# Kernel tuning notes

Measured on AMD Instinct MI355X. Metric: run time of the kernel, lower is better.

Reference implementation:

```python
import jax, jax.numpy as jnp
import numpy as np

B, T = 32, 2048            # batch, seq_len
V = 16                     # vocab_size
H = 256                    # hidden_size
NV = V + 2                 # embedding rows (padding_idx=0 + vocab + delimiter)
NO = V + 1                 # head output size


def setup_inputs() -> dict:
    key = jax.random.key(0)
    ks = jax.random.split(key, 8)
    s = 1.0 / np.sqrt(H).astype(np.float32)
    tokens = jax.random.randint(ks[0], (B, T), 0, NV)
    embed = jax.random.normal(ks[1], (NV, H), jnp.float32) * 0.02
    embed = embed.at[0].set(0.0)  # padding_idx=0
    # GRU params (PyTorch layout: gates [r|z|n] stacked on last dim)
    W_ih = jax.random.uniform(ks[2], (H, 3 * H), jnp.float32, -s, s)
    W_hh = jax.random.uniform(ks[3], (H, 3 * H), jnp.float32, -s, s)
    b_ih = jax.random.uniform(ks[4], (3 * H,), jnp.float32, -s, s)
    b_hh = jax.random.uniform(ks[5], (3 * H,), jnp.float32, -s, s)
    W_head = jax.random.uniform(ks[6], (H, NO), jnp.float32, -s, s)
    b_head = jax.random.uniform(ks[7], (NO,), jnp.float32, -s, s)
    return {"tokens": tokens, "embed": embed, "W_ih": W_ih, "W_hh": W_hh,
            "b_ih": b_ih, "b_hh": b_hh, "W_head": W_head, "b_head": b_head}


def _mogru_scan(x, W_ih, W_hh, b_ih, b_hh):
    # x: [B, T, H]. Precompute all input projections in one big GEMM.
    gi = x @ W_ih + b_ih                      # [B, T, 3H]
    gi_t = jnp.swapaxes(gi, 0, 1)             # [T, B, 3H] for scan
    h0 = jnp.zeros((x.shape[0], W_hh.shape[0]), x.dtype)

    def step(h, gi_step):
        gh = h @ W_hh + b_hh                  # [B, 3H]
        i_r, i_z, i_n = jnp.split(gi_step, 3, axis=-1)
        h_r, h_z, h_n = jnp.split(gh, 3, axis=-1)
        r = jax.nn.sigmoid(i_r + h_r)
        z = jax.nn.sigmoid(i_z + h_z)         # beta: retention gate
        n = jnp.tanh(i_n + r * h_n)
        h_new = (1.0 - z) * n + z * h
        return h_new, (h_new, z)

    h_last, (outs, betas) = jax.lax.scan(step, h0, gi_t)
    return jnp.swapaxes(outs, 0, 1), h_last, jnp.swapaxes(betas, 0, 1)


def reference(tokens, embed, W_ih, W_hh, b_ih, b_hh, W_head, b_head):
    x = embed[tokens]                          # [B, T, H] embedding lookup
    output, _, betas = _mogru_scan(x, W_ih, W_hh, b_ih, b_hh)
    logits = output @ W_head + b_head          # [B, T, V+1]
    return logits, betas
```

## Files before the change

### kernel.cpp

```cpp
#include <hip/hip_runtime.h>

#define BB   32
#define TT   2048
#define HH   256
#define G3   768
#define NVOC 18
#define NOUT 17
#define LOGITS_ELEMS ((size_t)BB * TT * NOUT)

typedef _Float16 h2 __attribute__((ext_vector_type(2)));

__device__ __forceinline__ float bf1(unsigned short u){
  union{unsigned int i; float f;} v; v.i = ((unsigned int)u) << 16; return v.f;
}
__device__ __forceinline__ unsigned short f2bf(float f){
  union{float f; unsigned int i;} v; v.f = f;
  unsigned int lsb = (v.i >> 16) & 1u;
  v.i += 0x7fffu + lsb;
  return (unsigned short)(v.i >> 16);
}
__device__ __forceinline__ float bflo(unsigned int u){
  union{unsigned int i; float f;} v; v.i = u << 16; return v.f;
}
__device__ __forceinline__ float bfhi(unsigned int u){
  union{unsigned int i; float f;} v; v.i = u & 0xffff0000u; return v.f;
}

__device__ __forceinline__ float ld1(const float* p, size_t i){ return p[i]; }
__device__ __forceinline__ float ld1(const unsigned short* p, size_t i){ return bf1(p[i]); }

__device__ __forceinline__ bool detect_f32(const void* W_ih_raw){
  const unsigned short* u = (const unsigned short*)W_ih_raw;
  bool big = false;
  #pragma unroll
  for (int i = 0; i < 64; i++){
    float v = bf1(u[i]);
    big |= !(v >= -0.25f && v <= 0.25f);
  }
  return big;
}

#if __has_builtin(__builtin_amdgcn_fdot2)
#define FDOT2(a,b,c) __builtin_amdgcn_fdot2((a),(b),(c),false)
#else
#define FDOT2(a,b,c) ((c) + (float)(a).x*(float)(b).x + (float)(a).y*(float)(b).y)
#endif

template<typename T>
__device__ __forceinline__ void prep_body(const T* W_hh, unsigned int* Wp){
  unsigned int e = blockIdx.x * 256 + threadIdx.x;
  unsigned int c = e & 3, tmp = e >> 2;
  unsigned int tid = tmp & 511, f = tmp >> 9;
  unsigned int m = (f << 2) | c;
  unsigned int g = m >> 6, kk = m & 63;
  unsigned int u = tid >> 1, q = tid & 1;
  unsigned int col = g * 256 + u;
  unsigned int k0 = q * 128 + kk * 2;
  float lo = ld1(W_hh, (size_t)k0 * G3 + col);
  float hi = ld1(W_hh, (size_t)(k0 + 1) * G3 + col);
  h2 t; t.x = (_Float16)lo; t.y = (_Float16)hi;
  Wp[e] = __builtin_bit_cast(unsigned int, t);
}

__global__ __launch_bounds__(256) void k_prep(
    const void* __restrict__ W_hh, const void* __restrict__ W_ih,
    unsigned int* __restrict__ Wp)
{
  if (detect_f32(W_ih)) prep_body<float>((const float*)W_hh, Wp);
  else                  prep_body<unsigned short>((const unsigned short*)W_hh, Wp);
}

template<typename T>
__device__ __forceinline__ void proj_body(const T* embed, const T* W_ih,
                                          const T* b_ih, const T* b_hh,
                                          float* proj, float* bb){
  __shared__ float s_e[HH];
  int v = blockIdx.x, j = threadIdx.x;
  if (j < HH) s_e[j] = ld1(embed, (size_t)v * HH + j);
  if (v == 0) bb[j] = ld1(b_hh, (size_t)j);
  __syncthreads();
  float acc = ld1(b_ih, (size_t)j);
  if (j < 2 * HH) acc += ld1(b_hh, (size_t)j);
  #pragma unroll 8
  for (int k = 0; k < HH; k++)
    acc += s_e[k] * ld1(W_ih, (size_t)k * G3 + j);
  proj[(size_t)v * G3 + j] = acc;
}

__global__ __launch_bounds__(768) void k_proj(
    const void* __restrict__ embed, const void* __restrict__ W_ih,
    const void* __restrict__ b_ih, const void* __restrict__ b_hh,
    float* __restrict__ proj, float* __restrict__ bb)
{
  if (detect_f32(W_ih))
    proj_body<float>((const float*)embed, (const float*)W_ih,
                     (const float*)b_ih, (const float*)b_hh, proj, bb);
  else
    proj_body<unsigned short>((const unsigned short*)embed,
                              (const unsigned short*)W_ih,
                              (const unsigned short*)b_ih,
                              (const unsigned short*)b_hh, proj, bb);
}

#define SPROJ_PAD 6656

__global__ __launch_bounds__(512, 1)
__attribute__((amdgpu_waves_per_eu(1, 2)))
void k_scan(
    const int*          __restrict__ tokens,
    const unsigned int* __restrict__ Wp,
    const float*        __restrict__ bb,
    const void*         __restrict__ W_ih,
    const float*        __restrict__ proj,
    unsigned short*     __restrict__ outs,
    void*               __restrict__ d_out_base)
{
  __shared__ float s_proj[NVOC * G3 + SPROJ_PAD];
  __shared__ __align__(16) unsigned int s_hA[136];
  __shared__ __align__(16) unsigned int s_hB[136];

  const bool f32m = detect_f32(W_ih);
  const int b   = blockIdx.x;
  const int tid = threadIdx.x;
  const int u   = tid >> 1;
  const int q   = tid & 1;

  for (int i = tid; i < NVOC * G3; i += 512) s_proj[i] = proj[i];

  h2 w[192];
  {
    const float4* wp4 = (const float4*)Wp;
    #pragma unroll
    for (int f = 0; f < 48; f++) {
      float4 v = wp4[(size_t)f * 512 + tid];
      w[4*f+0] = __builtin_bit_cast(h2, v.x);
      w[4*f+1] = __builtin_bit_cast(h2, v.y);
      w[4*f+2] = __builtin_bit_cast(h2, v.z);
      w[4*f+3] = __builtin_bit_cast(h2, v.w);
    }
  }
  const float bbn = bb[2 * HH + u];

  if (tid < 136) s_hA[tid] = 0u;
  float h_old = 0.f;

  const int* tptr = tokens + (size_t)b * TT;
  int tok = tptr[0];
  unsigned short* orow   = outs + (size_t)b * TT * HH + u;
  unsigned short* brow_b = (unsigned short*)d_out_base + LOGITS_ELEMS
                           + (size_t)b * TT * HH + u;
  float*          brow_f = (float*)d_out_base + LOGITS_ELEMS
                           + (size_t)b * TT * HH + u;

  __syncthreads();

#define STEP(T, RB, WB)                                                      \
  {                                                                          \
    int tok_cur = tok;                                                       \
    tok = ((T) + 1 < TT) ? tptr[(T) + 1] : 0;                                \
    const float* pj = s_proj + tok_cur * G3;                                 \
    float gir = pj[u], giz = pj[HH + u], gin = pj[2*HH + u];                 \
    const int4* hp = (const int4*)(RB);                                      \
    float ar[4] = {0.f,0.f,0.f,0.f};                                         \
    float az[4] = {0.f,0.f,0.f,0.f};                                         \
    float an[4] = {0.f,0.f,0.f,0.f};                                         \
    _Pragma("unroll")                                                        \
    for (int i = 0; i < 16; i++) {                                           \
      int4 hv = hp[q * 17 + i];                                              \
      h2 x0 = __builtin_bit_cast(h2, hv.x);                                  \
      h2 x1 = __builtin_bit_cast(h2, hv.y);                                  \
      h2 x2 = __builtin_bit_cast(h2, hv.z);                                  \
      h2 x3 = __builtin_bit_cast(h2, hv.w);                                  \
      ar[0] = FDOT2(w[4*i+0],       x0, ar[0]);                              \
      ar[1] = FDOT2(w[4*i+1],       x1, ar[1]);                              \
      ar[2] = FDOT2(w[4*i+2],       x2, ar[2]);                              \
      ar[3] = FDOT2(w[4*i+3],       x3, ar[3]);                              \
      az[0] = FDOT2(w[64+4*i+0],    x0, az[0]);                              \
      az[1] = FDOT2(w[64+4*i+1],    x1, az[1]);                              \
      az[2] = FDOT2(w[64+4*i+2],    x2, az[2]);                              \
      az[3] = FDOT2(w[64+4*i+3],    x3, az[3]);                              \
      an[0] = FDOT2(w[128+4*i+0],   x0, an[0]);                              \
      an[1] = FDOT2(w[128+4*i+1],   x1, an[1]);                              \
      an[2] = FDOT2(w[128+4*i+2],   x2, an[2]);                              \
      an[3] = FDOT2(w[128+4*i+3],   x3, an[3]);                              \
    }                                                                        \
    float gr = (ar[0] + ar[1]) + (ar[2] + ar[3]);                            \
    float gz = (az[0] + az[1]) + (az[2] + az[3]);                            \
    float gn = (an[0] + an[1]) + (an[2] + an[3]);                            \
    gr += __shfl_xor(gr, 1);                                                 \
    gz += __shfl_xor(gz, 1);                                                 \
    gn += __shfl_xor(gn, 1);                                                 \
    float r = 1.f / (1.f + __expf(-(gir + gr)));                             \
    float z = 1.f / (1.f + __expf(-(giz + gz)));                             \
    float x = gin + r * (gn + bbn);                                          \
    x = fminf(fmaxf(x, -15.f), 15.f);                                        \
    float ex = __expf(2.f * x);                                              \
    float n = (ex - 1.f) / (ex + 1.f);                                       \
    float hn = (1.f - z) * n + z * h_old;                                    \
    h_old = hn;                                                              \
    if (q == 0) {                                                            \
      ((_Float16*)(WB))[(u >> 7) * 136 + (u & 127)] = (_Float16)hn;          \
      orow[(size_t)(T) * HH] = f2bf(hn);                                     \
    } else {                                                                 \
      if (f32m) brow_f[(size_t)(T) * HH] = z;                                \
      else      brow_b[(size_t)(T) * HH] = f2bf(z);                          \
    }                                                                        \
    __syncthreads();                                                         \
  }

  for (int t = 0; t < TT; t += 2) {
    STEP(t,     s_hA, s_hB)
    STEP(t + 1, s_hB, s_hA)
  }
#undef STEP
}

template<typename T>
__device__ __forceinline__ void stage_head(const T* W_head, const T* b_head,
                                           float* s_w, float* s_b, int tid){
  for (int i = tid; i < NOUT * HH; i += 256) {
    int o = i / HH, k = i - o * HH;
    s_w[i] = ld1(W_head, (size_t)k * NOUT + o);
  }
  if (tid < NOUT) s_b[tid] = ld1(b_head, (size_t)tid);
}

__global__ __launch_bounds__(256) void k_head(
    const unsigned short* __restrict__ outs,
    const void* __restrict__ W_head,
    const void* __restrict__ b_head,
    const void* __restrict__ W_ih,
    void* __restrict__ logits_out)
{
  __shared__ float s_w[NOUT * HH];
  __shared__ float s_b[NOUT];
  const bool f32m = detect_f32(W_ih);
  const int tid = threadIdx.x;

  if (f32m) stage_head<float>((const float*)W_head, (const float*)b_head,
                              s_w, s_b, tid);
  else      stage_head<unsigned short>((const unsigned short*)W_head,
                                       (const unsigned short*)b_head,
                                       s_w, s_b, tid);
  __syncthreads();

  size_t gid = (size_t)blockIdx.x * 256 + tid;
  if (gid >= LOGITS_ELEMS) return;
  int o = (int)(gid % NOUT);
  size_t row = gid / NOUT;

  const uint4* xp = (const uint4*)(outs + row * HH);
  const float* wv = s_w + o * HH;
  float a0 = 0.f, a1 = 0.f, a2 = 0.f, a3 = 0.f;
  #pragma unroll 8
  for (int kk = 0; kk < 32; kk++) {
    uint4 u = xp[kk];
    int kb = kk * 8;
    a0 += bflo(u.x) * wv[kb+0] + bfhi(u.x) * wv[kb+1];
    a1 += bflo(u.y) * wv[kb+2] + bfhi(u.y) * wv[kb+3];
    a2 += bflo(u.z) * wv[kb+4] + bfhi(u.z) * wv[kb+5];
    a3 += bflo(u.w) * wv[kb+6] + bfhi(u.w) * wv[kb+7];
  }
  float val = ((a0 + a1) + (a2 + a3)) + s_b[o];
  if (f32m) ((float*)logits_out)[gid] = val;
  else      ((unsigned short*)logits_out)[gid] = f2bf(val);
}

extern "C" void kernel_launch(void* const* d_in, const int* in_sizes, int n_in,
                              void* d_out, int out_size, void* d_ws, size_t ws_size,
                              hipStream_t stream)
{
  const int* tokens = (const int*)d_in[0];
  const void* embed  = d_in[1];
  const void* W_ih   = d_in[2];
  const void* W_hh   = d_in[3];
  const void* b_ih   = d_in[4];
  const void* b_hh   = d_in[5];
  const void* W_head = d_in[6];
  const void* b_head = d_in[7];

  char* ws = (char*)d_ws;
  float*          proj = (float*)ws;
  float*          bb   = (float*)(ws + 55296);
  unsigned int*   Wp   = (unsigned int*)(ws + 55296 + 3072);
  unsigned short* outs = (unsigned short*)(ws + 55296 + 3072 + 393216);

  k_prep<<<384, 256, 0, stream>>>(W_hh, W_ih, Wp);
  k_proj<<<NVOC, G3, 0, stream>>>(embed, W_ih, b_ih, b_hh, proj, bb);
  k_scan<<<BB, 512, 0, stream>>>(tokens, Wp, bb, W_ih, proj, outs, d_out);
  k_head<<<(int)((LOGITS_ELEMS + 255) / 256), 256, 0, stream>>>(
      outs, W_head, b_head, W_ih, d_out);
}
```

Before: 2.793 ms.

## Split each hidden unit's recurrent dot product across four lanes with 1024-thread scan blocks

The GRU scan kernel now uses 1024 threads per batch row, with four lanes per hidden unit instead of two. Each lane holds 96 packed fp16 weight pairs instead of 192 and covers a quarter of the K dimension. Partial sums are combined with two xor shuffles, and the k_prep weight packing and the shared h buffer padding are changed to match the new layout. This halves per-thread serial FDOT2 work and register pressure on the latency-bound recurrent step. In exchange the block-wide barrier spans 16 waves, there is an extra shuffle stage, and each accumulator is now a single serial chain rather than four independent ones.

```diff
diff --git a/kernel.cpp b/kernel.cpp
--- a/kernel.cpp
+++ b/kernel.cpp
@@ -48,18 +48,18 @@
 
 template<typename T>
 __device__ __forceinline__ void prep_body(const T* W_hh, unsigned int* Wp){
-  unsigned int e = blockIdx.x * 256 + threadIdx.x;
-  unsigned int c = e & 3, tmp = e >> 2;
-  unsigned int tid = tmp & 511, f = tmp >> 9;
-  unsigned int m = (f << 2) | c;
-  unsigned int g = m >> 6, kk = m & 63;
-  unsigned int u = tid >> 1, q = tid & 1;
+  unsigned int E = blockIdx.x * 256 + threadIdx.x;
+  unsigned int c = E & 3, idx4 = E >> 2;
+  unsigned int tid = idx4 & 1023, f = idx4 >> 10;
+  unsigned int m = 4 * f + c;
+  unsigned int g = m >> 5, kk = m & 31;
+  unsigned int u = tid >> 2, q = tid & 3;
   unsigned int col = g * 256 + u;
-  unsigned int k0 = q * 128 + kk * 2;
+  unsigned int k0 = q * 64 + 2 * kk;
   float lo = ld1(W_hh, (size_t)k0 * G3 + col);
   float hi = ld1(W_hh, (size_t)(k0 + 1) * G3 + col);
   h2 t; t.x = (_Float16)lo; t.y = (_Float16)hi;
-  Wp[e] = __builtin_bit_cast(unsigned int, t);
+  Wp[E] = __builtin_bit_cast(unsigned int, t);
 }
 
 __global__ __launch_bounds__(256) void k_prep(
@@ -102,10 +102,10 @@
                               (const unsigned short*)b_hh, proj, bb);
 }
 
-#define SPROJ_PAD 6656
-
-__global__ __launch_bounds__(512, 1)
-__attribute__((amdgpu_waves_per_eu(1, 2)))
+#define SPROJ_PAD 6400
+
+__global__ __launch_bounds__(1024)
+__attribute__((amdgpu_waves_per_eu(4, 4)))
 void k_scan(
     const int*          __restrict__ tokens,
     const unsigned int* __restrict__ Wp,
@@ -116,23 +116,23 @@
     void*               __restrict__ d_out_base)
 {
   __shared__ float s_proj[NVOC * G3 + SPROJ_PAD];
-  __shared__ __align__(16) unsigned int s_hA[136];
-  __shared__ __align__(16) unsigned int s_hB[136];
+  __shared__ __align__(16) unsigned int s_hA[144];
+  __shared__ __align__(16) unsigned int s_hB[144];
 
   const bool f32m = detect_f32(W_ih);
   const int b   = blockIdx.x;
   const int tid = threadIdx.x;
-  const int u   = tid >> 1;
-  const int q   = tid & 1;
-
-  for (int i = tid; i < NVOC * G3; i += 512) s_proj[i] = proj[i];
-
-  h2 w[192];
+  const int u   = tid >> 2;
+  const int q   = tid & 3;
+
+  for (int i = tid; i < NVOC * G3; i += 1024) s_proj[i] = proj[i];
+
+  h2 w[96];
   {
     const float4* wp4 = (const float4*)Wp;
     #pragma unroll
-    for (int f = 0; f < 48; f++) {
-      float4 v = wp4[(size_t)f * 512 + tid];
+    for (int f = 0; f < 24; f++) {
+      float4 v = wp4[(size_t)f * 1024 + tid];
       w[4*f+0] = __builtin_bit_cast(h2, v.x);
       w[4*f+1] = __builtin_bit_cast(h2, v.y);
       w[4*f+2] = __builtin_bit_cast(h2, v.z);
@@ -141,7 +141,7 @@
   }
   const float bbn = bb[2 * HH + u];
 
-  if (tid < 136) s_hA[tid] = 0u;
+  if (tid < 144) s_hA[tid] = 0u;
   float h_old = 0.f;
 
   const int* tptr = tokens + (size_t)b * TT;
@@ -161,47 +161,42 @@
     const float* pj = s_proj + tok_cur * G3;                                 \
     float gir = pj[u], giz = pj[HH + u], gin = pj[2*HH + u];                 \
     const int4* hp = (const int4*)(RB);                                      \
-    float ar[4] = {0.f,0.f,0.f,0.f};                                         \
-    float az[4] = {0.f,0.f,0.f,0.f};                                         \
-    float an[4] = {0.f,0.f,0.f,0.f};                                         \
+    float ar = 0.f, az = 0.f, an = 0.f;                                      \
     _Pragma("unroll")                                                        \
-    for (int i = 0; i < 16; i++) {                                           \
-      int4 hv = hp[q * 17 + i];                                              \
+    for (int i = 0; i < 8; i++) {                                            \
+      int4 hv = hp[q * 9 + i];                                               \
       h2 x0 = __builtin_bit_cast(h2, hv.x);                                  \
       h2 x1 = __builtin_bit_cast(h2, hv.y);                                  \
       h2 x2 = __builtin_bit_cast(h2, hv.z);                                  \
       h2 x3 = __builtin_bit_cast(h2, hv.w);                                  \
-      ar[0] = FDOT2(w[4*i+0],       x0, ar[0]);                              \
-      ar[1] = FDOT2(w[4*i+1],       x1, ar[1]);                              \
-      ar[2] = FDOT2(w[4*i+2],       x2, ar[2]);                              \
-      ar[3] = FDOT2(w[4*i+3],       x3, ar[3]);                              \
-      az[0] = FDOT2(w[64+4*i+0],    x0, az[0]);                              \
-      az[1] = FDOT2(w[64+4*i+1],    x1, az[1]);                              \
-      az[2] = FDOT2(w[64+4*i+2],    x2, az[2]);                              \
-      az[3] = FDOT2(w[64+4*i+3],    x3, az[3]);                              \
-      an[0] = FDOT2(w[128+4*i+0],   x0, an[0]);                              \
-      an[1] = FDOT2(w[128+4*i+1],   x1, an[1]);                              \
-      an[2] = FDOT2(w[128+4*i+2],   x2, an[2]);                              \
-      an[3] = FDOT2(w[128+4*i+3],   x3, an[3]);                              \
+      ar = FDOT2(w[4*i+0],      x0, ar);                                     \
+      ar = FDOT2(w[4*i+1],      x1, ar);                                     \
+      ar = FDOT2(w[4*i+2],      x2, ar);                                     \
+      ar = FDOT2(w[4*i+3],      x3, ar);                                     \
+      az = FDOT2(w[32+4*i+0],   x0, az);                                     \
+      az = FDOT2(w[32+4*i+1],   x1, az);                                     \
+      az = FDOT2(w[32+4*i+2],   x2, az);                                     \
+      az = FDOT2(w[32+4*i+3],   x3, az);                                     \
+      an = FDOT2(w[64+4*i+0],   x0, an);                                     \
+      an = FDOT2(w[64+4*i+1],   x1, an);                                     \
+      an = FDOT2(w[64+4*i+2],   x2, an);                                     \
+      an = FDOT2(w[64+4*i+3],   x3, an);                                     \
     }                                                                        \
-    float gr = (ar[0] + ar[1]) + (ar[2] + ar[3]);                            \
-    float gz = (az[0] + az[1]) + (az[2] + az[3]);                            \
-    float gn = (an[0] + an[1]) + (an[2] + an[3]);                            \
-    gr += __shfl_xor(gr, 1);                                                 \
-    gz += __shfl_xor(gz, 1);                                                 \
-    gn += __shfl_xor(gn, 1);                                                 \
-    float r = 1.f / (1.f + __expf(-(gir + gr)));                             \
-    float z = 1.f / (1.f + __expf(-(giz + gz)));                             \
-    float x = gin + r * (gn + bbn);                                          \
+    ar += __shfl_xor(ar, 1);  ar += __shfl_xor(ar, 2);                       \
+    az += __shfl_xor(az, 1);  az += __shfl_xor(az, 2);                       \
+    an += __shfl_xor(an, 1);  an += __shfl_xor(an, 2);                       \
+    float r = 1.f / (1.f + __expf(-(gir + ar)));                             \
+    float z = 1.f / (1.f + __expf(-(giz + az)));                             \
+    float x = gin + r * (an + bbn);                                          \
     x = fminf(fmaxf(x, -15.f), 15.f);                                        \
     float ex = __expf(2.f * x);                                              \
     float n = (ex - 1.f) / (ex + 1.f);                                       \
     float hn = (1.f - z) * n + z * h_old;                                    \
     h_old = hn;                                                              \
     if (q == 0) {                                                            \
-      ((_Float16*)(WB))[(u >> 7) * 136 + (u & 127)] = (_Float16)hn;          \
+      ((_Float16*)(WB))[(u >> 6) * 72 + (u & 63)] = (_Float16)hn;            \
       orow[(size_t)(T) * HH] = f2bf(hn);                                     \
-    } else {                                                                 \
+    } else if (q == 1) {                                                     \
       if (f32m) brow_f[(size_t)(T) * HH] = z;                                \
       else      brow_b[(size_t)(T) * HH] = f2bf(z);                          \
     }                                                                        \
@@ -287,7 +282,7 @@
 
   k_prep<<<384, 256, 0, stream>>>(W_hh, W_ih, Wp);
   k_proj<<<NVOC, G3, 0, stream>>>(embed, W_ih, b_ih, b_hh, proj, bb);
-  k_scan<<<BB, 512, 0, stream>>>(tokens, Wp, bb, W_ih, proj, outs, d_out);
+  k_scan<<<BB, 1024, 0, stream>>>(tokens, Wp, bb, W_ih, proj, outs, d_out);
   k_head<<<(int)((LOGITS_ELEMS + 255) / 256), 256, 0, stream>>>(
       outs, W_head, b_head, W_ih, d_out);
 }
```

Measured after the change: 3.517 ms. +25.9%, slower.
